# Optimization experiments

Hardware: AMD Instinct MI355X
Metric: run time of the kernel (lower is better)

Reference implementation:

```python
import jax, jax.numpy as jnp
import numpy as np

T, H, I, E, K, G, TG = 8192, 2048, 1024, 64, 8, 8, 4
ROUTED_SCALE = 2.5


def setup_inputs() -> dict:
    key = jax.random.key(0)
    ks = jax.random.split(key, 7)
    s = 0.02  # weight init scale
    return {
        "hidden_states": jax.random.normal(ks[0], (T, H), jnp.float32),
        "gate_w": jax.random.normal(ks[1], (E, H), jnp.float32) * s,
        "e_bias": jax.random.normal(ks[2], (E,), jnp.float32) * s,
        "w_gate_up": jax.random.normal(ks[3], (E, H, 2 * I), jnp.float32) * s,
        "w_down": jax.random.normal(ks[4], (E, I, H), jnp.float32) * s,
        "shared_gate_up": jax.random.normal(ks[5], (H, 2 * I), jnp.float32) * s,
        "shared_down": jax.random.normal(ks[6], (I, H), jnp.float32) * s,
    }


def silu_and_mul(x):
    g, u = jnp.split(x, 2, axis=-1)
    return jax.nn.silu(g) * u


def grouped_topk(router_logits, e_bias):
    # sigmoid scoring with e_score_correction_bias (DeepSeek-V3 / GLM4-MoE style)
    scores = jax.nn.sigmoid(router_logits)            # [T, E]
    scores_for_choice = scores + e_bias[None, :]
    # group score = sum of top-2 biased scores in each group
    grp = scores_for_choice.reshape(-1, G, E // G)
    group_scores = jax.lax.top_k(grp, 2)[0].sum(-1)   # [T, G]
    _, gidx = jax.lax.top_k(group_scores, TG)         # [T, TG]
    tok = jnp.arange(scores.shape[0])[:, None]
    group_mask = jnp.zeros_like(group_scores, dtype=bool).at[tok, gidx].set(True)
    expert_mask = jnp.repeat(group_mask, E // G, axis=-1)  # [T, E]
    masked = jnp.where(expert_mask, scores_for_choice, -jnp.inf)
    _, topk_ids = jax.lax.top_k(masked, K)            # [T, K]
    # combine weights come from the *unbiased* sigmoid scores
    topk_w = jnp.take_along_axis(scores, topk_ids, axis=-1)
    topk_w = topk_w / jnp.sum(topk_w, axis=-1, keepdims=True)  # renormalize
    return topk_w, topk_ids


def reference(hidden_states, gate_w, e_bias, w_gate_up, w_down,
              shared_gate_up, shared_down):
    x = hidden_states                                  # [T, H]
    # gate runs in fp32
    router_logits = x.astype(jnp.float32) @ gate_w.T   # [T, E]
    topk_w, topk_ids = grouped_topk(router_logits, e_bias)

    # shared expert MLP
    shared_out = silu_and_mul(x @ shared_gate_up) @ shared_down  # [T, H]

    # dense [T, E] combine matrix (top-k sparse in values)
    tok = jnp.arange(x.shape[0])[:, None]
    route = jnp.zeros((x.shape[0], E), x.dtype).at[tok, topk_ids].set(
        topk_w.astype(x.dtype))

    # grouped expert GEMMs via scan over experts (bounds peak memory)
    def body(acc, params):
        w1, w2, rw = params                            # [H,2I], [I,H], [T]
        y = silu_and_mul(x @ w1) @ w2                  # [T, H]
        return acc + rw[:, None] * y, None

    acc0 = jnp.zeros_like(x)
    routed_out, _ = jax.lax.scan(body, acc0, (w_gate_up, w_down, route.T))

    return routed_out * ROUTED_SCALE + shared_out
```

## Files before the change

### kernel.cpp

```cpp
#include <hip/hip_runtime.h>
#include <stdint.h>

#define T_TOK 8192
#define HDIM  2048
#define IDIM  1024
#define NEXP  64
#define KTOP  8
#define TGRP  4
#define TKTOT (T_TOK*KTOP)
#define MAXITEMS 4096
#define RSCALE 2.5f

typedef __attribute__((ext_vector_type(8))) short short8;
typedef __attribute__((ext_vector_type(4))) float f32x4;

#define VMCNT(n) asm volatile("s_waitcnt vmcnt(" #n ")" ::: "memory")
#define BARRIER() asm volatile("s_barrier" ::: "memory")

__device__ __forceinline__ float bf2f(uint16_t u) {
    union { unsigned i; float f; } v; v.i = ((unsigned)u) << 16; return v.f;
}
__device__ __forceinline__ uint16_t f2bf(float f) {
    union { float f; unsigned i; } v; v.f = f;
    unsigned r = (v.i + 0x7FFFu + ((v.i >> 16) & 1u)) >> 16;
    return (uint16_t)r;
}
__device__ __forceinline__ void gload_lds16(const void* g, void* l) {
    __builtin_amdgcn_global_load_lds(
        (const __attribute__((address_space(1))) void*)g,
        (__attribute__((address_space(3))) void*)l, 16, 0, 0);
}
__device__ __forceinline__ int imin(int a, int b) { return a < b ? a : b; }

__global__ __launch_bounds__(256) void k_router(
    const float* __restrict__ x, const float* __restrict__ gw,
    const float* __restrict__ ebias,
    int* __restrict__ topk_ids, float* __restrict__ topk_w,
    int* __restrict__ counts)
{
    __shared__ float xs[16][132];
    __shared__ float wsb[64][133];
    __shared__ float sc[16][65];
    __shared__ float su[16][65];
    const int tid = threadIdx.x;
    const int e = tid & 63;
    const int tg = tid >> 6;
    const long tblk = (long)blockIdx.x * 16;

    float acc0 = 0.f, acc1 = 0.f, acc2 = 0.f, acc3 = 0.f;
    for (int ch = 0; ch < 16; ++ch) {
        const int h0 = ch << 7;
        for (int i = tid; i < 512; i += 256) {
            int r = i >> 5, c4 = (i & 31) << 2;
            float4 v = *(const float4*)(x + (tblk + r) * HDIM + h0 + c4);
            *(float4*)&xs[r][c4] = v;
        }
        for (int i = tid; i < 8192; i += 256) {
            int r = i >> 7, c = i & 127;
            wsb[r][c] = gw[(long)r * HDIM + h0 + c];
        }
        __syncthreads();
        #pragma unroll 8
        for (int hh = 0; hh < 128; ++hh) {
            float wv = wsb[e][hh];
            acc0 += xs[tg][hh] * wv;
            acc1 += xs[tg + 4][hh] * wv;
            acc2 += xs[tg + 8][hh] * wv;
            acc3 += xs[tg + 12][hh] * wv;
        }
        __syncthreads();
    }
    const float be = ebias[e];
    {
        float s;
        s = 1.f / (1.f + expf(-acc0)); su[tg][e] = s;      sc[tg][e] = s + be;
        s = 1.f / (1.f + expf(-acc1)); su[tg + 4][e] = s;  sc[tg + 4][e] = s + be;
        s = 1.f / (1.f + expf(-acc2)); su[tg + 8][e] = s;  sc[tg + 8][e] = s + be;
        s = 1.f / (1.f + expf(-acc3)); su[tg + 12][e] = s; sc[tg + 12][e] = s + be;
    }
    __syncthreads();
    if (tid < 16) {
        const int t = tid;
        float gs[8];
        #pragma unroll
        for (int g = 0; g < 8; ++g) {
            float m1 = -1e30f, m2 = -1e30f;
            #pragma unroll
            for (int j = 0; j < 8; ++j) {
                float v = sc[t][g * 8 + j];
                if (v > m1) { m2 = m1; m1 = v; } else if (v > m2) { m2 = v; }
            }
            gs[g] = m1 + m2;
        }
        int selmask = 0;
        #pragma unroll
        for (int it = 0; it < TGRP; ++it) {
            float best = -1e30f; int bg = 0;
            #pragma unroll
            for (int g = 0; g < 8; ++g)
                if (!((selmask >> g) & 1) && gs[g] > best) { best = gs[g]; bg = g; }
            selmask |= (1 << bg);
        }
        unsigned long long chosen = 0ull;
        int ids[KTOP]; float wv[KTOP]; float wsum = 0.f;
        #pragma unroll
        for (int it = 0; it < KTOP; ++it) {
            float best = -1e30f; int bi = 0;
            for (int ee = 0; ee < 64; ++ee) {
                if (((selmask >> (ee >> 3)) & 1) && !((chosen >> ee) & 1ull)) {
                    float v = sc[t][ee];
                    if (v > best) { best = v; bi = ee; }
                }
            }
            chosen |= (1ull << bi);
            ids[it] = bi; wv[it] = su[t][bi]; wsum += wv[it];
        }
        const float inv = 1.f / wsum;
        #pragma unroll
        for (int k = 0; k < KTOP; ++k) {
            topk_ids[(tblk + t) * KTOP + k] = ids[k];
            topk_w[(tblk + t) * KTOP + k] = wv[k] * inv;
            atomicAdd(&counts[ids[k]], 1);
        }
    }
}

__global__ __launch_bounds__(64) void k_scan4(
    const int* __restrict__ counts, int* offsets, int* cursor,
    int* __restrict__ it_r0, int* __restrict__ it_end,
    int* __restrict__ it_e, int* __restrict__ it_n0,
    int* __restrict__ nitems, int* __restrict__ qctl)
{
    const int e = threadIdx.x;
    const int c = counts[e];
    int pre = c;
    #pragma unroll
    for (int d = 1; d < 64; d <<= 1) {
        int v = __shfl_up(pre, d, 64);
        if (e >= d) pre += v;
    }
    const int offE = pre - c;
    offsets[e] = offE; cursor[e] = offE;
    const int ntl = (c + 255) >> 8;
    int ipre = ntl;
    #pragma unroll
    for (int d = 1; d < 64; d <<= 1) {
        int v = __shfl_up(ipre, d, 64);
        if (e >= d) ipre += v;
    }
    const int ibase = (ipre - ntl) * 8;
    for (int t = 0; t < ntl; ++t)
        for (int p = 0; p < 8; ++p) {
            int idx = ibase + t * 8 + p;
            it_r0[idx] = offE + t * 256;
            it_end[idx] = offE + c;
            it_e[idx] = e;
            it_n0[idx] = p << 8;
        }
    const int totTl = __shfl(ipre, 63, 64);
    const int NI = totTl * 8;
    if (e == 63) *nitems = NI;
    if (e < 8) {
        int s  = (int)(((long)e * NI) / 8);
        int en = (int)(((long)(e + 1) * NI) / 8);
        qctl[e] = s;       qctl[8 + e]  = en;
        qctl[16 + e] = s;  qctl[24 + e] = en;
    }
}

__global__ __launch_bounds__(256) void k_scatter(
    const int* __restrict__ topk_ids, int* cursor,
    int* __restrict__ perm_token, int* __restrict__ slot_of)
{
    int i = blockIdx.x * 256 + threadIdx.x;
    if (i >= TKTOT) return;
    int e = topk_ids[i];
    int pos = atomicAdd(&cursor[e], 1);
    perm_token[pos] = i >> 3;
    slot_of[i] = pos;
}

__global__ __launch_bounds__(256) void k_cvt_bf16(
    const float* __restrict__ in, uint16_t* __restrict__ outp, long n4)
{
    long i = (long)blockIdx.x * 256 + threadIdx.x;
    if (i >= n4) return;
    float4 v = *(const float4*)(in + i * 4);
    uint64_t pk = (uint64_t)f2bf(v.x) | ((uint64_t)f2bf(v.y) << 16)
                | ((uint64_t)f2bf(v.z) << 32) | ((uint64_t)f2bf(v.w) << 48);
    *(uint64_t*)(outp + i * 4) = pk;
}

template<bool INTER>
__global__ __launch_bounds__(256) void k_transpose2(
    const float* __restrict__ src, uint16_t* __restrict__ dst,
    int R, int C, long sStride, long dStride)
{
    __shared__ float tile[64][65];
    const int c0 = blockIdx.x << 6, r0 = blockIdx.y << 6, s = blockIdx.z;
    const float* S = src + (long)s * sStride;
    uint16_t* D = dst + (long)s * dStride;
    const int lc = (threadIdx.x & 15) << 2;
    const int lr = threadIdx.x >> 4;
    #pragma unroll
    for (int p = 0; p < 4; ++p) {
        int y = lr + p * 16;
        float4 v = *(const float4*)(S + (long)(r0 + y) * C + c0 + lc);
        tile[y][lc] = v.x; tile[y][lc + 1] = v.y;
        tile[y][lc + 2] = v.z; tile[y][lc + 3] = v.w;
    }
    __syncthreads();
    const int wc = threadIdx.x >> 3;
    const int wx = (threadIdx.x & 7) << 3;
    #pragma unroll
    for (int p = 0; p < 2; ++p) {
        int c = wc + p * 32;
        short8 v;
        #pragma unroll
        for (int j = 0; j < 8; ++j) v[j] = (short)f2bf(tile[wx + j][c]);
        int cg = c0 + c;
        int rd = INTER ? (((cg & (IDIM - 1)) << 1) + (cg >> 10)) : cg;
        *(short8*)(D + (long)rd * R + r0 + wx) = v;
    }
}

template<bool GATEUP, bool ROUTED>
__global__ __launch_bounds__(512, 2) void k_gemm9(
    const uint16_t* __restrict__ A, const uint16_t* __restrict__ Bw,
    void* __restrict__ OutP,
    const int* __restrict__ perm_token,
    const int* __restrict__ it_r0, const int* __restrict__ it_end,
    const int* __restrict__ it_e, const int* __restrict__ it_n0,
    const int* __restrict__ nitems, int* __restrict__ qcur,
    int Kd, long expStride)
{
    __shared__ char ldsb[4 * 32768];
    __shared__ int s_item;
    const int tid = threadIdx.x, lane = tid & 63, wid = tid >> 6;
    const int wm = wid >> 2, wn = wid & 3;

    const int rchunk = lane >> 2;
    const int swzS = ((lane & 3) ^ ((lane >> 3) & 3)) << 3;
    const int swzR = ((lane >> 4) ^ ((lane >> 1) & 3)) << 4;
    const int aoff = (wm * 128 + (lane & 15)) * 64 + swzR;
    const int boff = (wn * 64 + (lane & 15)) * 64 + swzR;
    const int dstA0 = (wid * 2) * 1024;
    const int dstA1 = (wid * 2 + 1) * 1024;

    const int nKt = Kd >> 5;
    const int xcd = (int)(blockIdx.x & 7);
    const int myEnd = ROUTED ? qcur[8 + xcd] : 0;
    int* myCur = qcur + xcd;

    for (;;) {
        int row0, end, n0; long eoff;
        if (ROUTED) {
            __syncthreads();
            if (tid == 0) s_item = atomicAdd(myCur, 1);
            __syncthreads();
            const int it = s_item;
            if (it >= myEnd) break;
            row0 = it_r0[it]; end = it_end[it]; n0 = it_n0[it];
            eoff = (long)it_e[it] * expStride;
        } else {
            row0 = (int)(blockIdx.x >> 3) << 8;
            end = row0 + 256;
            n0 = (int)(blockIdx.x & 7) << 8;
            eoff = 0;
        }

        const uint16_t *pa0, *pa1, *pb0, *pb1;
        {
            int r0l = wid * 32 + rchunk;
            int r1l = wid * 32 + 16 + rchunk;
            int ra0 = row0 + r0l, ra1 = row0 + r1l;
            if (ROUTED) { ra0 = imin(ra0, end - 1); ra1 = imin(ra1, end - 1); }
            long ga0 = (GATEUP && ROUTED) ? (long)perm_token[ra0] : (long)ra0;
            long ga1 = (GATEUP && ROUTED) ? (long)perm_token[ra1] : (long)ra1;
            pa0 = A + ga0 * Kd + swzS;
            pa1 = A + ga1 * Kd + swzS;
            pb0 = Bw + eoff + (long)(n0 + r0l) * Kd + swzS;
            pb1 = Bw + eoff + (long)(n0 + r1l) * Kd + swzS;
        }

        f32x4 acc[8][4];
        #pragma unroll
        for (int f = 0; f < 8; ++f)
            #pragma unroll
            for (int g = 0; g < 4; ++g) { f32x4 z = {0.f,0.f,0.f,0.f}; acc[f][g] = z; }

        #pragma unroll
        for (int j = 0; j < 3; ++j) {
            char* bb = ldsb + j * 32768;
            gload_lds16(pa0 + (j << 5), bb + dstA0);
            gload_lds16(pa1 + (j << 5), bb + dstA1);
            gload_lds16(pb0 + (j << 5), bb + 16384 + dstA0);
            gload_lds16(pb1 + (j << 5), bb + 16384 + dstA1);
        }

        for (int kt = 0; kt < nKt; ++kt) {
            const char* bb = ldsb + (kt & 3) * 32768;
            char* bs = ldsb + ((kt + 3) & 3) * 32768;
            const bool st = (kt + 3) < nKt;

            if (kt + 2 < nKt)      VMCNT(8);
            else if (kt + 1 < nKt) VMCNT(4);
            else                   VMCNT(0);
            BARRIER();

            short8 fa0 = *(const short8*)(bb + aoff);
            short8 fa1 = *(const short8*)(bb + aoff + 1024);
            short8 fa2 = *(const short8*)(bb + aoff + 2048);
            short8 fa3 = *(const short8*)(bb + aoff + 3072);
            short8 fb0 = *(const short8*)(bb + 16384 + boff);
            short8 fb1 = *(const short8*)(bb + 16384 + boff + 1024);
            short8 fb2 = *(const short8*)(bb + 16384 + boff + 2048);
            short8 fb3 = *(const short8*)(bb + 16384 + boff + 3072);
            if (st) {
                gload_lds16(pa0 + ((kt + 3) << 5), bs + dstA0);
                gload_lds16(pa1 + ((kt + 3) << 5), bs + dstA1);
            }
            BARRIER();
            __builtin_amdgcn_s_setprio(1);
            acc[0][0] = __builtin_amdgcn_mfma_f32_16x16x32_bf16(fa0, fb0, acc[0][0], 0, 0, 0);
            acc[0][1] = __builtin_amdgcn_mfma_f32_16x16x32_bf16(fa0, fb1, acc[0][1], 0, 0, 0);
            acc[0][2] = __builtin_amdgcn_mfma_f32_16x16x32_bf16(fa0, fb2, acc[0][2], 0, 0, 0);
            acc[0][3] = __builtin_amdgcn_mfma_f32_16x16x32_bf16(fa0, fb3, acc[0][3], 0, 0, 0);
            acc[1][0] = __builtin_amdgcn_mfma_f32_16x16x32_bf16(fa1, fb0, acc[1][0], 0, 0, 0);
            acc[1][1] = __builtin_amdgcn_mfma_f32_16x16x32_bf16(fa1, fb1, acc[1][1], 0, 0, 0);
            acc[1][2] = __builtin_amdgcn_mfma_f32_16x16x32_bf16(fa1, fb2, acc[1][2], 0, 0, 0);
            acc[1][3] = __builtin_amdgcn_mfma_f32_16x16x32_bf16(fa1, fb3, acc[1][3], 0, 0, 0);
            acc[2][0] = __builtin_amdgcn_mfma_f32_16x16x32_bf16(fa2, fb0, acc[2][0], 0, 0, 0);
            acc[2][1] = __builtin_amdgcn_mfma_f32_16x16x32_bf16(fa2, fb1, acc[2][1], 0, 0, 0);
            acc[2][2] = __builtin_amdgcn_mfma_f32_16x16x32_bf16(fa2, fb2, acc[2][2], 0, 0, 0);
            acc[2][3] = __builtin_amdgcn_mfma_f32_16x16x32_bf16(fa2, fb3, acc[2][3], 0, 0, 0);
            acc[3][0] = __builtin_amdgcn_mfma_f32_16x16x32_bf16(fa3, fb0, acc[3][0], 0, 0, 0);
            acc[3][1] = __builtin_amdgcn_mfma_f32_16x16x32_bf16(fa3, fb1, acc[3][1], 0, 0, 0);
            acc[3][2] = __builtin_amdgcn_mfma_f32_16x16x32_bf16(fa3, fb2, acc[3][2], 0, 0, 0);
            acc[3][3] = __builtin_amdgcn_mfma_f32_16x16x32_bf16(fa3, fb3, acc[3][3], 0, 0, 0);
            __builtin_amdgcn_s_setprio(0);

            short8 fa4 = *(const short8*)(bb + aoff + 4096);
            short8 fa5 = *(const short8*)(bb + aoff + 5120);
            short8 fa6 = *(const short8*)(bb + aoff + 6144);
            short8 fa7 = *(const short8*)(bb + aoff + 7168);
            if (st) {
                gload_lds16(pb0 + ((kt + 3) << 5), bs + 16384 + dstA0);
                gload_lds16(pb1 + ((kt + 3) << 5), bs + 16384 + dstA1);
            }
            BARRIER();
            __builtin_amdgcn_s_setprio(1);
            acc[4][0] = __builtin_amdgcn_mfma_f32_16x16x32_bf16(fa4, fb0, acc[4][0], 0, 0, 0);
            acc[4][1] = __builtin_amdgcn_mfma_f32_16x16x32_bf16(fa4, fb1, acc[4][1], 0, 0, 0);
            acc[4][2] = __builtin_amdgcn_mfma_f32_16x16x32_bf16(fa4, fb2, acc[4][2], 0, 0, 0);
            acc[4][3] = __builtin_amdgcn_mfma_f32_16x16x32_bf16(fa4, fb3, acc[4][3], 0, 0, 0);
            acc[5][0] = __builtin_amdgcn_mfma_f32_16x16x32_bf16(fa5, fb0, acc[5][0], 0, 0, 0);
            acc[5][1] = __builtin_amdgcn_mfma_f32_16x16x32_bf16(fa5, fb1, acc[5][1], 0, 0, 0);
            acc[5][2] = __builtin_amdgcn_mfma_f32_16x16x32_bf16(fa5, fb2, acc[5][2], 0, 0, 0);
            acc[5][3] = __builtin_amdgcn_mfma_f32_16x16x32_bf16(fa5, fb3, acc[5][3], 0, 0, 0);
            acc[6][0] = __builtin_amdgcn_mfma_f32_16x16x32_bf16(fa6, fb0, acc[6][0], 0, 0, 0);
            acc[6][1] = __builtin_amdgcn_mfma_f32_16x16x32_bf16(fa6, fb1, acc[6][1], 0, 0, 0);
            acc[6][2] = __builtin_amdgcn_mfma_f32_16x16x32_bf16(fa6, fb2, acc[6][2], 0, 0, 0);
            acc[6][3] = __builtin_amdgcn_mfma_f32_16x16x32_bf16(fa6, fb3, acc[6][3], 0, 0, 0);
            acc[7][0] = __builtin_amdgcn_mfma_f32_16x16x32_bf16(fa7, fb0, acc[7][0], 0, 0, 0);
            acc[7][1] = __builtin_amdgcn_mfma_f32_16x16x32_bf16(fa7, fb1, acc[7][1], 0, 0, 0);
            acc[7][2] = __builtin_amdgcn_mfma_f32_16x16x32_bf16(fa7, fb2, acc[7][2], 0, 0, 0);
            acc[7][3] = __builtin_amdgcn_mfma_f32_16x16x32_bf16(fa7, fb3, acc[7][3], 0, 0, 0);
            __builtin_amdgcn_s_setprio(0);
        }

        const int colb = n0 + wn * 64 + (lane & 15);
        const int rowbase = row0 + wm * 128 + ((lane >> 4) << 2);
        if (GATEUP) {
            uint16_t* Oact = (uint16_t*)OutP;
            const bool evenl = ((lane & 1) == 0);
            #pragma unroll
            for (int f = 0; f < 8; ++f)
                #pragma unroll
                for (int g = 0; g < 4; ++g) {
                    f32x4 v = acc[f][g];
                    #pragma unroll
                    for (int r = 0; r < 4; ++r) {
                        float gg = v[r];
                        float uu = __shfl_xor(gg, 1, 64);
                        int row = rowbase + f * 16 + r;
                        if (evenl && (!ROUTED || row < end)) {
                            int jcol = (colb + g * 16) >> 1;
                            float sg = gg / (1.f + __expf(-gg));
                            Oact[(long)row * IDIM + jcol] = f2bf(sg * uu);
                        }
                    }
                }
        } else if (ROUTED) {
            uint16_t* Y = (uint16_t*)OutP;
            #pragma unroll
            for (int f = 0; f < 8; ++f)
                #pragma unroll
                for (int g = 0; g < 4; ++g) {
                    f32x4 v = acc[f][g];
                    #pragma unroll
                    for (int r = 0; r < 4; ++r) {
                        int row = rowbase + f * 16 + r;
                        if (row < end)
                            Y[(long)row * HDIM + colb + g * 16] = f2bf(v[r]);
                    }
                }
        } else {
            float* O = (float*)OutP;
            #pragma unroll
            for (int f = 0; f < 8; ++f)
                #pragma unroll
                for (int g = 0; g < 4; ++g) {
                    f32x4 v = acc[f][g];
                    #pragma unroll
                    for (int r = 0; r < 4; ++r) {
                        int row = rowbase + f * 16 + r;
                        O[(long)row * HDIM + colb + g * 16] = v[r];
                    }
                }
        }
        if (!ROUTED) break;
    }
}

__global__ __launch_bounds__(256) void k_combine(
    float* __restrict__ out, const uint16_t* __restrict__ ybuf,
    const int* __restrict__ slot_of, const float* __restrict__ topk_w)
{
    __shared__ int sl[KTOP];
    __shared__ float sw[KTOP];
    const int t = blockIdx.x, tid = threadIdx.x;
    if (tid < KTOP) {
        sl[tid] = slot_of[t * KTOP + tid];
        sw[tid] = topk_w[t * KTOP + tid] * RSCALE;
    }
    __syncthreads();
    const int h0 = tid << 3;
    float* orow = out + (long)t * HDIM + h0;
    float4 v0 = *(const float4*)(orow);
    float4 v1 = *(const float4*)(orow + 4);
    float a[8] = { v0.x, v0.y, v0.z, v0.w, v1.x, v1.y, v1.z, v1.w };
    #pragma unroll
    for (int k = 0; k < KTOP; ++k) {
        const uint16_t* yr = ybuf + (long)sl[k] * HDIM + h0;
        short8 y = *(const short8*)yr;
        float w = sw[k];
        #pragma unroll
        for (int j = 0; j < 8; ++j)
            a[j] += w * bf2f((uint16_t)y[j]);
    }
    v0.x = a[0]; v0.y = a[1]; v0.z = a[2]; v0.w = a[3];
    v1.x = a[4]; v1.y = a[5]; v1.z = a[6]; v1.w = a[7];
    *(float4*)(orow) = v0;
    *(float4*)(orow + 4) = v1;
}

extern "C" void kernel_launch(void* const* d_in, const int* in_sizes, int n_in,
                              void* d_out, int out_size, void* d_ws, size_t ws_size,
                              hipStream_t stream)
{
    const float* x  = (const float*)d_in[0];
    const float* gw = (const float*)d_in[1];
    const float* eb = (const float*)d_in[2];
    const float* w1 = (const float*)d_in[3];
    const float* w2 = (const float*)d_in[4];
    const float* s1 = (const float*)d_in[5];
    const float* s2 = (const float*)d_in[6];
    float* out = (float*)d_out;
    char* ws = (char*)d_ws;

    size_t off = 0;
    auto take = [&](size_t b) { size_t r = off; off += (b + 255) & ~(size_t)255; return r; };
    const size_t oXBF = take((size_t)T_TOK * HDIM * 2);
    const size_t oACT = take((size_t)TKTOT * IDIM * 2);
    const size_t oASH = take((size_t)T_TOK * IDIM * 2);
    const size_t oW1T = take((size_t)NEXP * 2048 * 2048 * 2);
    const size_t oW2T = take((size_t)NEXP * 2048 * 1024 * 2);
    const size_t oS1T = take((size_t)2048 * 2048 * 2);
    const size_t oS2T = take((size_t)2048 * 1024 * 2);
    const size_t oTKI = take((size_t)TKTOT * 4);
    const size_t oTKW = take((size_t)TKTOT * 4);
    const size_t oSLT = take((size_t)TKTOT * 4);
    const size_t oPRM = take((size_t)TKTOT * 4);
    const size_t oCTL = take(1024);
    const size_t oOFS = take(256);
    const size_t oCUR = take(256);
    const size_t oNT  = take(256);
    const size_t oIR  = take(MAXITEMS * 4);
    const size_t oIE  = take(MAXITEMS * 4);
    const size_t oIX  = take(MAXITEMS * 4);
    const size_t oIN  = take(MAXITEMS * 4);
    (void)ws_size; (void)in_sizes; (void)n_in; (void)out_size;

    uint16_t* xbf  = (uint16_t*)(ws + oXBF);
    uint16_t* act  = (uint16_t*)(ws + oACT);
    uint16_t* ash  = (uint16_t*)(ws + oASH);
    uint16_t* w1t  = (uint16_t*)(ws + oW1T);
    uint16_t* ybuf = (uint16_t*)(ws + oW1T);
    uint16_t* w2t  = (uint16_t*)(ws + oW2T);
    uint16_t* s1t  = (uint16_t*)(ws + oS1T);
    uint16_t* s2t  = (uint16_t*)(ws + oS2T);
    int*   tki  = (int*)(ws + oTKI);
    float* tkw  = (float*)(ws + oTKW);
    int*   slot = (int*)(ws + oSLT);
    int*   prm  = (int*)(ws + oPRM);
    int*   ctl  = (int*)(ws + oCTL);
    int*   ofs  = (int*)(ws + oOFS);
    int*   cur  = (int*)(ws + oCUR);
    int*   nt   = (int*)(ws + oNT);
    int*   ir0  = (int*)(ws + oIR);
    int*   iend = (int*)(ws + oIE);
    int*   ie   = (int*)(ws + oIX);
    int*   in0  = (int*)(ws + oIN);
    int*   qctl = ctl + 64;

    hipMemsetAsync(ws + oCTL, 0, 1024, stream);

    k_router<<<T_TOK / 16, 256, 0, stream>>>(x, gw, eb, tki, tkw, ctl);
    k_scan4<<<1, 64, 0, stream>>>(ctl, ofs, cur, ir0, iend, ie, in0, nt, qctl);
    k_scatter<<<TKTOT / 256, 256, 0, stream>>>(tki, cur, prm, slot);

    k_cvt_bf16<<<(T_TOK * HDIM / 4 + 255) / 256, 256, 0, stream>>>(x, xbf, (long)T_TOK * HDIM / 4);
    k_transpose2<true ><<<dim3(32, 32, NEXP), 256, 0, stream>>>(w1, w1t, 2048, 2048,
        (long)2048 * 2048, (long)2048 * 2048);
    k_transpose2<false><<<dim3(32, 16, NEXP), 256, 0, stream>>>(w2, w2t, 1024, 2048,
        (long)1024 * 2048, (long)2048 * 1024);
    k_transpose2<true ><<<dim3(32, 32, 1), 256, 0, stream>>>(s1, s1t, 2048, 2048, 0, 0);
    k_transpose2<false><<<dim3(32, 16, 1), 256, 0, stream>>>(s2, s2t, 1024, 2048, 0, 0);

    k_gemm9<true, false><<<dim3(256), 512, 0, stream>>>(
        xbf, s1t, ash, nullptr, nullptr, nullptr, nullptr, nullptr, nullptr, qctl, 2048, 0);
    k_gemm9<true, true><<<dim3(256), 512, 0, stream>>>(
        xbf, w1t, act, prm, ir0, iend, ie, in0, nt, qctl, 2048, (long)2048 * 2048);
    k_gemm9<false, false><<<dim3(256), 512, 0, stream>>>(
        ash, s2t, out, nullptr, nullptr, nullptr, nullptr, nullptr, nullptr, qctl, 1024, 0);
    k_gemm9<false, true><<<dim3(256), 512, 0, stream>>>(
        act, w2t, ybuf, nullptr, ir0, iend, ie, in0, nt, qctl + 16, 1024, (long)2048 * 1024);

    k_combine<<<T_TOK, 256, 0, stream>>>(out, ybuf, slot, tkw);
}
```

Baseline: 2.130 ms.

## Treat shared expert as extra routed expert and fuse bf16 conversion into router

The shared expert MLP becomes a 65th expert, with its tokens appended as extra slots and work items. Its GEMMs are therefore scheduled by the same persistent grouped-GEMM launches instead of separate dense launches, and the transposes for shared weights are folded into the expert transpose grids. The fp32-to-bf16 conversion of activations moves into the router kernel, which already reads x, removing a separate pass. In exchange, the shared output is stored in bf16 in ybuf before combine, which loses precision compared with the previous fp32 output path. Routed and shared work also now compete within one queue.

```diff
diff --git a/kernel.cpp b/kernel.cpp
--- a/kernel.cpp
+++ b/kernel.cpp
@@ -8,6 +8,7 @@
 #define KTOP  8
 #define TGRP  4
 #define TKTOT (T_TOK*KTOP)
+#define NSLOT (TKTOT + T_TOK)
 #define MAXITEMS 4096
 #define RSCALE 2.5f
 
@@ -36,7 +37,7 @@
     const float* __restrict__ x, const float* __restrict__ gw,
     const float* __restrict__ ebias,
     int* __restrict__ topk_ids, float* __restrict__ topk_w,
-    int* __restrict__ counts)
+    int* __restrict__ counts, uint16_t* __restrict__ xbf)
 {
     __shared__ float xs[16][132];
     __shared__ float wsb[64][133];
@@ -54,6 +55,9 @@
             int r = i >> 5, c4 = (i & 31) << 2;
             float4 v = *(const float4*)(x + (tblk + r) * HDIM + h0 + c4);
             *(float4*)&xs[r][c4] = v;
+            uint64_t pk = (uint64_t)f2bf(v.x) | ((uint64_t)f2bf(v.y) << 16)
+                        | ((uint64_t)f2bf(v.z) << 32) | ((uint64_t)f2bf(v.w) << 48);
+            *(uint64_t*)(xbf + (tblk + r) * HDIM + h0 + c4) = pk;
         }
         for (int i = tid; i < 8192; i += 256) {
             int r = i >> 7, c = i & 127;
@@ -125,7 +129,7 @@
     }
 }
 
-__global__ __launch_bounds__(64) void k_scan4(
+__global__ __launch_bounds__(64) void k_scan6(
     const int* __restrict__ counts, int* offsets, int* cursor,
     int* __restrict__ it_r0, int* __restrict__ it_end,
     int* __restrict__ it_e, int* __restrict__ it_n0,
@@ -158,7 +162,17 @@
             it_n0[idx] = p << 8;
         }
     const int totTl = __shfl(ipre, 63, 64);
-    const int NI = totTl * 8;
+    int NI = totTl * 8;
+    if (e < 32) {
+        for (int p = 0; p < 8; ++p) {
+            int idx = NI + e * 8 + p;
+            it_r0[idx] = TKTOT + e * 256;
+            it_end[idx] = TKTOT + T_TOK;
+            it_e[idx] = 64;
+            it_n0[idx] = p << 8;
+        }
+    }
+    NI += 256;
     if (e == 63) *nitems = NI;
     if (e < 8) {
         int s  = (int)(((long)e * NI) / 8);
@@ -173,32 +187,25 @@
     int* __restrict__ perm_token, int* __restrict__ slot_of)
 {
     int i = blockIdx.x * 256 + threadIdx.x;
-    if (i >= TKTOT) return;
-    int e = topk_ids[i];
-    int pos = atomicAdd(&cursor[e], 1);
-    perm_token[pos] = i >> 3;
-    slot_of[i] = pos;
-}
-
-__global__ __launch_bounds__(256) void k_cvt_bf16(
-    const float* __restrict__ in, uint16_t* __restrict__ outp, long n4)
-{
-    long i = (long)blockIdx.x * 256 + threadIdx.x;
-    if (i >= n4) return;
-    float4 v = *(const float4*)(in + i * 4);
-    uint64_t pk = (uint64_t)f2bf(v.x) | ((uint64_t)f2bf(v.y) << 16)
-                | ((uint64_t)f2bf(v.z) << 32) | ((uint64_t)f2bf(v.w) << 48);
-    *(uint64_t*)(outp + i * 4) = pk;
+    if (i < TKTOT) {
+        int e = topk_ids[i];
+        int pos = atomicAdd(&cursor[e], 1);
+        perm_token[pos] = i >> 3;
+        slot_of[i] = pos;
+    } else if (i < NSLOT) {
+        perm_token[i] = i - TKTOT;
+    }
 }
 
 template<bool INTER>
-__global__ __launch_bounds__(256) void k_transpose2(
-    const float* __restrict__ src, uint16_t* __restrict__ dst,
+__global__ __launch_bounds__(256) void k_transpose3(
+    const float* __restrict__ src, const float* __restrict__ src2,
+    uint16_t* __restrict__ dst,
     int R, int C, long sStride, long dStride)
 {
     __shared__ float tile[64][65];
     const int c0 = blockIdx.x << 6, r0 = blockIdx.y << 6, s = blockIdx.z;
-    const float* S = src + (long)s * sStride;
+    const float* S = (s == NEXP) ? src2 : (src + (long)s * sStride);
     uint16_t* D = dst + (long)s * dStride;
     const int lc = (threadIdx.x & 15) << 2;
     const int lr = threadIdx.x >> 4;
@@ -224,14 +231,14 @@
     }
 }
 
-template<bool GATEUP, bool ROUTED>
-__global__ __launch_bounds__(512, 2) void k_gemm9(
+template<bool GATEUP>
+__global__ __launch_bounds__(512, 2) void k_gemm11(
     const uint16_t* __restrict__ A, const uint16_t* __restrict__ Bw,
     void* __restrict__ OutP,
     const int* __restrict__ perm_token,
     const int* __restrict__ it_r0, const int* __restrict__ it_end,
     const int* __restrict__ it_e, const int* __restrict__ it_n0,
-    const int* __restrict__ nitems, int* __restrict__ qcur,
+    int* __restrict__ qcur,
     int Kd, long expStride)
 {
     __shared__ char ldsb[4 * 32768];
@@ -249,34 +256,26 @@
 
     const int nKt = Kd >> 5;
     const int xcd = (int)(blockIdx.x & 7);
-    const int myEnd = ROUTED ? qcur[8 + xcd] : 0;
+    const int myEnd = qcur[8 + xcd];
     int* myCur = qcur + xcd;
 
     for (;;) {
-        int row0, end, n0; long eoff;
-        if (ROUTED) {
-            __syncthreads();
-            if (tid == 0) s_item = atomicAdd(myCur, 1);
-            __syncthreads();
-            const int it = s_item;
-            if (it >= myEnd) break;
-            row0 = it_r0[it]; end = it_end[it]; n0 = it_n0[it];
-            eoff = (long)it_e[it] * expStride;
-        } else {
-            row0 = (int)(blockIdx.x >> 3) << 8;
-            end = row0 + 256;
-            n0 = (int)(blockIdx.x & 7) << 8;
-            eoff = 0;
-        }
+        __syncthreads();
+        if (tid == 0) s_item = atomicAdd(myCur, 1);
+        __syncthreads();
+        const int it = s_item;
+        if (it >= myEnd) break;
+        const int row0 = it_r0[it], end = it_end[it], n0 = it_n0[it];
+        const long eoff = (long)it_e[it] * expStride;
 
         const uint16_t *pa0, *pa1, *pb0, *pb1;
         {
             int r0l = wid * 32 + rchunk;
             int r1l = wid * 32 + 16 + rchunk;
-            int ra0 = row0 + r0l, ra1 = row0 + r1l;
-            if (ROUTED) { ra0 = imin(ra0, end - 1); ra1 = imin(ra1, end - 1); }
-            long ga0 = (GATEUP && ROUTED) ? (long)perm_token[ra0] : (long)ra0;
-            long ga1 = (GATEUP && ROUTED) ? (long)perm_token[ra1] : (long)ra1;
+            int ra0 = imin(row0 + r0l, end - 1);
+            int ra1 = imin(row0 + r1l, end - 1);
+            long ga0 = GATEUP ? (long)perm_token[ra0] : (long)ra0;
+            long ga1 = GATEUP ? (long)perm_token[ra1] : (long)ra1;
             pa0 = A + ga0 * Kd + swzS;
             pa1 = A + ga1 * Kd + swzS;
             pb0 = Bw + eoff + (long)(n0 + r0l) * Kd + swzS;
@@ -384,14 +383,14 @@
                         float gg = v[r];
                         float uu = __shfl_xor(gg, 1, 64);
                         int row = rowbase + f * 16 + r;
-                        if (evenl && (!ROUTED || row < end)) {
+                        if (evenl && row < end) {
                             int jcol = (colb + g * 16) >> 1;
                             float sg = gg / (1.f + __expf(-gg));
                             Oact[(long)row * IDIM + jcol] = f2bf(sg * uu);
                         }
                     }
                 }
-        } else if (ROUTED) {
+        } else {
             uint16_t* Y = (uint16_t*)OutP;
             #pragma unroll
             for (int f = 0; f < 8; ++f)
@@ -405,21 +404,7 @@
                             Y[(long)row * HDIM + colb + g * 16] = f2bf(v[r]);
                     }
                 }
-        } else {
-            float* O = (float*)OutP;
-            #pragma unroll
-            for (int f = 0; f < 8; ++f)
-                #pragma unroll
-                for (int g = 0; g < 4; ++g) {
-                    f32x4 v = acc[f][g];
-                    #pragma unroll
-                    for (int r = 0; r < 4; ++r) {
-                        int row = rowbase + f * 16 + r;
-                        O[(long)row * HDIM + colb + g * 16] = v[r];
-                    }
-                }
-        }
-        if (!ROUTED) break;
+        }
     }
 }
 
@@ -436,10 +421,11 @@
     }
     __syncthreads();
     const int h0 = tid << 3;
-    float* orow = out + (long)t * HDIM + h0;
-    float4 v0 = *(const float4*)(orow);
-    float4 v1 = *(const float4*)(orow + 4);
-    float a[8] = { v0.x, v0.y, v0.z, v0.w, v1.x, v1.y, v1.z, v1.w };
+    const uint16_t* sr = ybuf + (long)(TKTOT + t) * HDIM + h0;
+    short8 sv = *(const short8*)sr;
+    float a[8];
+    #pragma unroll
+    for (int j = 0; j < 8; ++j) a[j] = bf2f((uint16_t)sv[j]);
     #pragma unroll
     for (int k = 0; k < KTOP; ++k) {
         const uint16_t* yr = ybuf + (long)sl[k] * HDIM + h0;
@@ -449,8 +435,9 @@
         for (int j = 0; j < 8; ++j)
             a[j] += w * bf2f((uint16_t)y[j]);
     }
-    v0.x = a[0]; v0.y = a[1]; v0.z = a[2]; v0.w = a[3];
-    v1.x = a[4]; v1.y = a[5]; v1.z = a[6]; v1.w = a[7];
+    float* orow = out + (long)t * HDIM + h0;
+    float4 v0 = { a[0], a[1], a[2], a[3] };
+    float4 v1 = { a[4], a[5], a[6], a[7] };
     *(float4*)(orow) = v0;
     *(float4*)(orow + 4) = v1;
 }
@@ -472,16 +459,13 @@
     size_t off = 0;
     auto take = [&](size_t b) { size_t r = off; off += (b + 255) & ~(size_t)255; return r; };
     const size_t oXBF = take((size_t)T_TOK * HDIM * 2);
-    const size_t oACT = take((size_t)TKTOT * IDIM * 2);
-    const size_t oASH = take((size_t)T_TOK * IDIM * 2);
-    const size_t oW1T = take((size_t)NEXP * 2048 * 2048 * 2);
-    const size_t oW2T = take((size_t)NEXP * 2048 * 1024 * 2);
-    const size_t oS1T = take((size_t)2048 * 2048 * 2);
-    const size_t oS2T = take((size_t)2048 * 1024 * 2);
+    const size_t oACT = take((size_t)NSLOT * IDIM * 2);
+    const size_t oW1T = take((size_t)(NEXP + 1) * 2048 * 2048 * 2);
+    const size_t oW2T = take((size_t)(NEXP + 1) * 2048 * 1024 * 2);
     const size_t oTKI = take((size_t)TKTOT * 4);
     const size_t oTKW = take((size_t)TKTOT * 4);
     const size_t oSLT = take((size_t)TKTOT * 4);
-    const size_t oPRM = take((size_t)TKTOT * 4);
+    const size_t oPRM = take((size_t)NSLOT * 4);
     const size_t oCTL = take(1024);
     const size_t oOFS = take(256);
     const size_t oCUR = take(256);
@@ -494,12 +478,9 @@
 
     uint16_t* xbf  = (uint16_t*)(ws + oXBF);
     uint16_t* act  = (uint16_t*)(ws + oACT);
-    uint16_t* ash  = (uint16_t*)(ws + oASH);
     uint16_t* w1t  = (uint16_t*)(ws + oW1T);
     uint16_t* ybuf = (uint16_t*)(ws + oW1T);
     uint16_t* w2t  = (uint16_t*)(ws + oW2T);
-    uint16_t* s1t  = (uint16_t*)(ws + oS1T);
-    uint16_t* s2t  = (uint16_t*)(ws + oS2T);
     int*   tki  = (int*)(ws + oTKI);
     float* tkw  = (float*)(ws + oTKW);
     int*   slot = (int*)(ws + oSLT);
@@ -516,26 +497,19 @@
 
     hipMemsetAsync(ws + oCTL, 0, 1024, stream);
 
-    k_router<<<T_TOK / 16, 256, 0, stream>>>(x, gw, eb, tki, tkw, ctl);
-    k_scan4<<<1, 64, 0, stream>>>(ctl, ofs, cur, ir0, iend, ie, in0, nt, qctl);
-    k_scatter<<<TKTOT / 256, 256, 0, stream>>>(tki, cur, prm, slot);
-
-    k_cvt_bf16<<<(T_TOK * HDIM / 4 + 255) / 256, 256, 0, stream>>>(x, xbf, (long)T_TOK * HDIM / 4);
-    k_transpose2<true ><<<dim3(32, 32, NEXP), 256, 0, stream>>>(w1, w1t, 2048, 2048,
+    k_router<<<T_TOK / 16, 256, 0, stream>>>(x, gw, eb, tki, tkw, ctl, xbf);
+    k_scan6<<<1, 64, 0, stream>>>(ctl, ofs, cur, ir0, iend, ie, in0, nt, qctl);
+    k_scatter<<<(NSLOT + 255) / 256, 256, 0, stream>>>(tki, cur, prm, slot);
+
+    k_transpose3<true ><<<dim3(32, 32, NEXP + 1), 256, 0, stream>>>(w1, s1, w1t, 2048, 2048,
         (long)2048 * 2048, (long)2048 * 2048);
-    k_transpose2<false><<<dim3(32, 16, NEXP), 256, 0, stream>>>(w2, w2t, 1024, 2048,
+    k_transpose3<false><<<dim3(32, 16, NEXP + 1), 256, 0, stream>>>(w2, s2, w2t, 1024, 2048,
         (long)1024 * 2048, (long)2048 * 1024);
-    k_transpose2<true ><<<dim3(32, 32, 1), 256, 0, stream>>>(s1, s1t, 2048, 2048, 0, 0);
-    k_transpose2<false><<<dim3(32, 16, 1), 256, 0, stream>>>(s2, s2t, 1024, 2048, 0, 0);
-
-    k_gemm9<true, false><<<dim3(256), 512, 0, stream>>>(
-        xbf, s1t, ash, nullptr, nullptr, nullptr, nullptr, nullptr, nullptr, qctl, 2048, 0);
-    k_gemm9<true, true><<<dim3(256), 512, 0, stream>>>(
-        xbf, w1t, act, prm, ir0, iend, ie, in0, nt, qctl, 2048, (long)2048 * 2048);
-    k_gemm9<false, false><<<dim3(256), 512, 0, stream>>>(
-        ash, s2t, out, nullptr, nullptr, nullptr, nullptr, nullptr, nullptr, qctl, 1024, 0);
-    k_gemm9<false, true><<<dim3(256), 512, 0, stream>>>(
-        act, w2t, ybuf, nullptr, ir0, iend, ie, in0, nt, qctl + 16, 1024, (long)2048 * 1024);
+
+    k_gemm11<true><<<dim3(256), 512, 0, stream>>>(
+        xbf, w1t, act, prm, ir0, iend, ie, in0, qctl, 2048, (long)2048 * 2048);
+    k_gemm11<false><<<dim3(256), 512, 0, stream>>>(
+        act, w2t, ybuf, prm, ir0, iend, ie, in0, qctl + 16, 1024, (long)2048 * 1024);
 
     k_combine<<<T_TOK, 256, 0, stream>>>(out, ybuf, slot, tkw);
 }
```

Result: no change. 2.113 ms (-0.8%).
